# Kernel optimization log

Hardware: AMD Instinct MI355X
Metric: run time of the kernel (lower is better)

Reference implementation:

```python
import jax, jax.numpy as jnp
import numpy as np

CODEBOOK_SIZE = 1024
EMBEDDING_DIM = 64


def setup_inputs() -> dict:
    key = jax.random.key(0)
    k_in, k_cb = jax.random.split(key)
    # latent feature (batch, embedding_dim, length)
    input = jax.random.normal(k_in, (16, EMBEDDING_DIM, 8192), dtype=jnp.float32)
    # learned codebook table (codebook_size, embedding_dim)
    codebook = jax.random.normal(k_cb, (CODEBOOK_SIZE, EMBEDDING_DIM), dtype=jnp.float32)
    return {"input": input, "codebook": codebook}


def reference(input, codebook):
    # input: (B, D, T); codebook: (K, D)
    B, D = input.shape[0], input.shape[1]
    spatial = input.shape[2:]
    # move embedding dim last and flatten tokens: (B*T, D)
    x = jnp.moveaxis(input, 1, -1).reshape(-1, D)
    x_sq = jnp.sum(x * x, axis=-1, keepdims=True)            # (N, 1)
    e_sq = jnp.sum(codebook * codebook, axis=-1)             # (K,)
    dist = x_sq - 2.0 * (x @ codebook.T) + e_sq[None, :]     # (N, K)
    indices = jnp.argmin(dist, axis=-1)                      # (N,)
    quantized = jnp.take(codebook, indices, axis=0)          # (N, D)
    # reshape back: output (B, D, *spatial), indices (B, *spatial)
    out = jnp.moveaxis(quantized.reshape((B,) + spatial + (D,)), -1, 1)
    idx = indices.reshape((B,) + spatial)
    return out, idx
```

## Files before the change

kernel.cpp:

```cpp
#include <hip/hip_runtime.h>
#include <float.h>

#define K_CODES 1024
#define DIM 64
#define T_LEN 8192
#define N_TOK 131072
#define LO_SCALE 2048.0f
#define NT_LDS 36
#define LDS_BYTES (NT_LDS * 4096 + 4096 + 2048)

typedef _Float16 half8 __attribute__((ext_vector_type(8)));
typedef float    f32x4 __attribute__((ext_vector_type(4)));

#define MFMA16(a, b, c) __builtin_amdgcn_mfma_f32_16x16x32_f16((a), (b), (c), 0, 0, 0)

__global__ void vq_prep(const float* __restrict__ cb,
                        _Float16* __restrict__ w,
                        float* __restrict__ wesq) {
    __shared__ float part[128];
    const int ct   = blockIdx.x;
    const int r    = threadIdx.x;
    const int halF = r >> 7;
    const int rr   = r & 127;
    const int q    = rr >> 4;
    const int code = rr & 15;

    const float* src = cb + (size_t)(ct * 16 + code) * DIM + q * 8;
    float4 v0 = *reinterpret_cast<const float4*>(src);
    float4 v1 = *reinterpret_cast<const float4*>(src + 4);
    float x[8] = {v0.x, v0.y, v0.z, v0.w, v1.x, v1.y, v1.z, v1.w};

    half8 o;
    float psum = 0.0f;
    #pragma unroll
    for (int j = 0; j < 8; ++j) {
        _Float16 h = (_Float16)x[j];
        o[j] = halF ? (_Float16)((x[j] - (float)h) * LO_SCALE) : h;
        psum = fmaf(x[j], x[j], psum);
    }
    *reinterpret_cast<half8*>(w + (size_t)ct * 2048 + halF * 1024 + q * 128 + code * 8) = o;

    if (halF == 0) part[rr] = psum;
    __syncthreads();
    if (r < 16) {
        float s = 0.0f;
        #pragma unroll
        for (int q2 = 0; q2 < 8; ++q2) s += part[q2 * 16 + r];
        wesq[ct * 16 + r] = s * LO_SCALE;
    }
}

__global__ __launch_bounds__(512, 2)
void vq_main(const float* __restrict__ in,
             const float* __restrict__ cb,
             const _Float16* __restrict__ w,
             const float* __restrict__ wesq,
             float* __restrict__ out) {
    extern __shared__ __align__(16) char smem[];
    _Float16* wlds  = (_Float16*)smem;
    float*    esq_s = (float*)(smem + NT_LDS * 4096);
    int*      idx_s = (int*)(smem + NT_LDS * 4096 + 4096);

    const int tid  = threadIdx.x;
    const int wave = tid >> 6;
    const int lane = tid & 63;
    const int lo4  = lane & 15;
    const int quad = lane >> 4;

    {
        const float4* gs = (const float4*)w;
        float4*       ls = (float4*)wlds;
        #pragma unroll 6
        for (int i = 0; i < NT_LDS * 4096 / 16 / 512; ++i)
            ls[i * 512 + tid] = gs[i * 512 + tid];
        #pragma unroll
        for (int k = tid; k < K_CODES; k += 512) esq_s[k] = wesq[k];
    }
    __syncthreads();

    const int strip = blockIdx.x * 512 + wave * 64;
    const int b  = strip >> 13;
    const int t0 = strip & 8191;

    const float* xin = in + (size_t)b * DIM * T_LEN + t0;
    half8 a_h[4][2], a_hs[4][2], a_l[4][2];
    #pragma unroll
    for (int mt = 0; mt < 4; ++mt) {
        #pragma unroll
        for (int s = 0; s < 2; ++s) {
            half8 hh, hs, ll;
            #pragma unroll
            for (int j = 0; j < 8; ++j) {
                const int d = s * 32 + quad * 8 + j;
                float xv = -2.0f * xin[(size_t)d * T_LEN + mt * 16 + lo4];
                _Float16 h = (_Float16)xv;
                hh[j] = h;
                hs[j] = (_Float16)((float)h * LO_SCALE);
                ll[j] = (_Float16)((xv - (float)h) * LO_SCALE);
            }
            a_h[mt][s] = hh;
            a_hs[mt][s] = hs;
            a_l[mt][s] = ll;
        }
    }

    float best[16];
    int   bidx[16];
    #pragma unroll
    for (int i = 0; i < 16; ++i) { best[i] = FLT_MAX; bidx[i] = 0; }

    const _Float16* wb_g = w    + (size_t)lane * 8;
    const _Float16* wb_l = wlds + (size_t)lane * 8;

    half8 Ah0, Ah1, Al0, Al1, Bh0, Bh1, Bl0, Bl1;
    float Ae, Be;
    auto loadB = [&](int ct, half8& h0, half8& h1, half8& l0, half8& l1, float& es) {
        if (ct < NT_LDS) {
            const _Float16* p = wb_l + (size_t)ct * 2048;
            h0 = *reinterpret_cast<const half8*>(p);
            h1 = *reinterpret_cast<const half8*>(p + 512);
            l0 = *reinterpret_cast<const half8*>(p + 1024);
            l1 = *reinterpret_cast<const half8*>(p + 1536);
        } else {
            const _Float16* p = wb_g + (size_t)ct * 2048;
            h0 = *reinterpret_cast<const half8*>(p);
            h1 = *reinterpret_cast<const half8*>(p + 512);
            l0 = *reinterpret_cast<const half8*>(p + 1024);
            l1 = *reinterpret_cast<const half8*>(p + 1536);
        }
        es = esq_s[ct * 16 + lo4];
    };
    auto step = [&](const half8& h0, const half8& h1, const half8& l0,
                    const half8& l1, float es, int ct) {
        const int code = ct * 16 + lo4;
        #pragma unroll
        for (int mt = 0; mt < 4; ++mt) {
            f32x4 c = {es, es, es, es};
            c = MFMA16(a_hs[mt][0], h0, c);
            c = MFMA16(a_hs[mt][1], h1, c);
            c = MFMA16(a_h[mt][0], l0, c);
            c = MFMA16(a_h[mt][1], l1, c);
            c = MFMA16(a_l[mt][0], h0, c);
            c = MFMA16(a_l[mt][1], h1, c);
            #pragma unroll
            for (int r = 0; r < 4; ++r) {
                float sc = c[r];
                const int i = mt * 4 + r;
                bool lt = sc < best[i];
                best[i] = lt ? sc : best[i];
                bidx[i] = lt ? code : bidx[i];
            }
        }
    };

    loadB(0, Ah0, Ah1, Al0, Al1, Ae);
    loadB(1, Bh0, Bh1, Bl0, Bl1, Be);
    for (int p = 0; p < 31; ++p) {
        step(Ah0, Ah1, Al0, Al1, Ae, 2 * p);
        loadB(2 * p + 2, Ah0, Ah1, Al0, Al1, Ae);
        step(Bh0, Bh1, Bl0, Bl1, Be, 2 * p + 1);
        loadB(2 * p + 3, Bh0, Bh1, Bl0, Bl1, Be);
    }
    step(Ah0, Ah1, Al0, Al1, Ae, 62);
    step(Bh0, Bh1, Bl0, Bl1, Be, 63);

    #pragma unroll
    for (int i = 0; i < 16; ++i) {
        float s = best[i];
        int  ix = bidx[i];
        #pragma unroll
        for (int off = 1; off < 16; off <<= 1) {
            float s2 = __shfl_xor(s, off, 64);
            int  ix2 = __shfl_xor(ix, off, 64);
            bool take = (s2 < s) || (s2 == s && ix2 < ix);
            s  = take ? s2 : s;
            ix = take ? ix2 : ix;
        }
        if (lo4 == 0) {
            idx_s[wave * 64 + (i >> 2) * 16 + quad * 4 + (i & 3)] = ix;
        }
    }
    __syncthreads();

    const int token = blockIdx.x * 512 + tid;
    const int tb = token >> 13;
    const int tt = token & 8191;
    const int my_idx = idx_s[tid];

    out[(size_t)N_TOK * DIM + token] = (float)my_idx;

    const float* crow = cb + (size_t)my_idx * DIM;
    float* outv = out + (size_t)tb * DIM * T_LEN + tt;
    #pragma unroll
    for (int d0 = 0; d0 < DIM; d0 += 4) {
        float4 v = *reinterpret_cast<const float4*>(crow + d0);
        outv[(size_t)(d0 + 0) * T_LEN] = v.x;
        outv[(size_t)(d0 + 1) * T_LEN] = v.y;
        outv[(size_t)(d0 + 2) * T_LEN] = v.z;
        outv[(size_t)(d0 + 3) * T_LEN] = v.w;
    }
}

extern "C" void kernel_launch(void* const* d_in, const int* in_sizes, int n_in,
                              void* d_out, int out_size, void* d_ws, size_t ws_size,
                              hipStream_t stream) {
    const float* in = (const float*)d_in[0];
    const float* cb = (const float*)d_in[1];
    float* out = (float*)d_out;

    _Float16* w   = (_Float16*)d_ws;
    float*   wesq = (float*)((char*)d_ws + 64 * 4096);

    static bool attr_done = false;
    if (!attr_done) {
        hipFuncSetAttribute(reinterpret_cast<const void*>(vq_main),
                            hipFuncAttributeMaxDynamicSharedMemorySize, LDS_BYTES);
        attr_done = true;
    }

    vq_prep<<<dim3(64), dim3(256), 0, stream>>>(cb, w, wesq);
    vq_main<<<dim3(N_TOK / 512), dim3(512), LDS_BYTES, stream>>>(in, cb, w, wesq, out);
}
```

Before: 132.9 us.

## Halve tokens per wave, shrink LDS codebook slice, raise occupancy to four blocks

Each wave now handles 32 tokens instead of 64, which halves the A-fragment and best/index register arrays. Launch bounds rise to 4 blocks per CU, and the LDS-resident codebook portion drops from 36 to 16 tiles so more blocks fit. The two independent MFMA accumulator chains are interleaved, and the gather/writeback is split across both halves of the block. In exchange the grid doubles, each codebook tile is reused over fewer tokens, and more B tiles are read from global/L2 rather than LDS.

```diff
diff --git a/kernel.cpp b/kernel.cpp
--- a/kernel.cpp
+++ b/kernel.cpp
@@ -6,8 +6,8 @@
 #define T_LEN 8192
 #define N_TOK 131072
 #define LO_SCALE 2048.0f
-#define NT_LDS 36
-#define LDS_BYTES (NT_LDS * 4096 + 4096 + 2048)
+#define NT_LDS 16
+#define LDS_BYTES (NT_LDS * 4096 + 4096 + 1024)
 
 typedef _Float16 half8 __attribute__((ext_vector_type(8)));
 typedef float    f32x4 __attribute__((ext_vector_type(4)));
@@ -50,7 +50,7 @@
     }
 }
 
-__global__ __launch_bounds__(512, 2)
+__global__ __launch_bounds__(512, 4)
 void vq_main(const float* __restrict__ in,
              const float* __restrict__ cb,
              const _Float16* __restrict__ w,
@@ -70,22 +70,21 @@
     {
         const float4* gs = (const float4*)w;
         float4*       ls = (float4*)wlds;
-        #pragma unroll 6
+        #pragma unroll
         for (int i = 0; i < NT_LDS * 4096 / 16 / 512; ++i)
             ls[i * 512 + tid] = gs[i * 512 + tid];
-        #pragma unroll
         for (int k = tid; k < K_CODES; k += 512) esq_s[k] = wesq[k];
     }
     __syncthreads();
 
-    const int strip = blockIdx.x * 512 + wave * 64;
+    const int strip = blockIdx.x * 256 + wave * 32;
     const int b  = strip >> 13;
     const int t0 = strip & 8191;
 
     const float* xin = in + (size_t)b * DIM * T_LEN + t0;
-    half8 a_h[4][2], a_hs[4][2], a_l[4][2];
-    #pragma unroll
-    for (int mt = 0; mt < 4; ++mt) {
+    half8 a_h[2][2], a_hs[2][2], a_l[2][2];
+    #pragma unroll
+    for (int mt = 0; mt < 2; ++mt) {
         #pragma unroll
         for (int s = 0; s < 2; ++s) {
             half8 hh, hs, ll;
@@ -104,10 +103,10 @@
         }
     }
 
-    float best[16];
-    int   bidx[16];
-    #pragma unroll
-    for (int i = 0; i < 16; ++i) { best[i] = FLT_MAX; bidx[i] = 0; }
+    float best[8];
+    int   bidx[8];
+    #pragma unroll
+    for (int i = 0; i < 8; ++i) { best[i] = FLT_MAX; bidx[i] = 0; }
 
     const _Float16* wb_g = w    + (size_t)lane * 8;
     const _Float16* wb_l = wlds + (size_t)lane * 8;
@@ -133,18 +132,25 @@
     auto step = [&](const half8& h0, const half8& h1, const half8& l0,
                     const half8& l1, float es, int ct) {
         const int code = ct * 16 + lo4;
-        #pragma unroll
-        for (int mt = 0; mt < 4; ++mt) {
-            f32x4 c = {es, es, es, es};
-            c = MFMA16(a_hs[mt][0], h0, c);
-            c = MFMA16(a_hs[mt][1], h1, c);
-            c = MFMA16(a_h[mt][0], l0, c);
-            c = MFMA16(a_h[mt][1], l1, c);
-            c = MFMA16(a_l[mt][0], h0, c);
-            c = MFMA16(a_l[mt][1], h1, c);
+        f32x4 c0 = {es, es, es, es}, c1 = {es, es, es, es};
+        c0 = MFMA16(a_hs[0][0], h0, c0);
+        c1 = MFMA16(a_hs[1][0], h0, c1);
+        c0 = MFMA16(a_hs[0][1], h1, c0);
+        c1 = MFMA16(a_hs[1][1], h1, c1);
+        c0 = MFMA16(a_h[0][0], l0, c0);
+        c1 = MFMA16(a_h[1][0], l0, c1);
+        c0 = MFMA16(a_h[0][1], l1, c0);
+        c1 = MFMA16(a_h[1][1], l1, c1);
+        c0 = MFMA16(a_l[0][0], h0, c0);
+        c1 = MFMA16(a_l[1][0], h0, c1);
+        c0 = MFMA16(a_l[0][1], h1, c0);
+        c1 = MFMA16(a_l[1][1], h1, c1);
+        f32x4 cc[2] = {c0, c1};
+        #pragma unroll
+        for (int mt = 0; mt < 2; ++mt) {
             #pragma unroll
             for (int r = 0; r < 4; ++r) {
-                float sc = c[r];
+                float sc = cc[mt][r];
                 const int i = mt * 4 + r;
                 bool lt = sc < best[i];
                 best[i] = lt ? sc : best[i];
@@ -165,7 +171,7 @@
     step(Bh0, Bh1, Bl0, Bl1, Be, 63);
 
     #pragma unroll
-    for (int i = 0; i < 16; ++i) {
+    for (int i = 0; i < 8; ++i) {
         float s = best[i];
         int  ix = bidx[i];
         #pragma unroll
@@ -177,22 +183,25 @@
             ix = take ? ix2 : ix;
         }
         if (lo4 == 0) {
-            idx_s[wave * 64 + (i >> 2) * 16 + quad * 4 + (i & 3)] = ix;
+            idx_s[wave * 32 + (i >> 2) * 16 + quad * 4 + (i & 3)] = ix;
         }
     }
     __syncthreads();
 
-    const int token = blockIdx.x * 512 + tid;
+    const int tok_l = tid & 255;
+    const int half_ = tid >> 8;
+    const int token = blockIdx.x * 256 + tok_l;
     const int tb = token >> 13;
     const int tt = token & 8191;
-    const int my_idx = idx_s[tid];
-
-    out[(size_t)N_TOK * DIM + token] = (float)my_idx;
-
-    const float* crow = cb + (size_t)my_idx * DIM;
-    float* outv = out + (size_t)tb * DIM * T_LEN + tt;
-    #pragma unroll
-    for (int d0 = 0; d0 < DIM; d0 += 4) {
+    const int my_idx = idx_s[tok_l];
+
+    if (half_ == 0)
+        out[(size_t)N_TOK * DIM + token] = (float)my_idx;
+
+    const float* crow = cb + (size_t)my_idx * DIM + half_ * 32;
+    float* outv = out + (size_t)tb * DIM * T_LEN + (size_t)(half_ * 32) * T_LEN + tt;
+    #pragma unroll
+    for (int d0 = 0; d0 < 32; d0 += 4) {
         float4 v = *reinterpret_cast<const float4*>(crow + d0);
         outv[(size_t)(d0 + 0) * T_LEN] = v.x;
         outv[(size_t)(d0 + 1) * T_LEN] = v.y;
@@ -219,5 +228,5 @@
     }
 
     vq_prep<<<dim3(64), dim3(256), 0, stream>>>(cb, w, wesq);
-    vq_main<<<dim3(N_TOK / 512), dim3(512), LDS_BYTES, stream>>>(in, cb, w, wesq, out);
+    vq_main<<<dim3(N_TOK / 256), dim3(512), LDS_BYTES, stream>>>(in, cb, w, wesq, out);
 }
```

After: 132.1 us. No clear change (-0.6%).
